# Performance work log

Hardware: AMD Instinct MI355X
Metric: run time of the kernel (lower is better)

## Reference

```python
import jax, jax.numpy as jnp
import numpy as np

B, NF, T, N = 64, 64, 8192, 1024  # batch, n_formants, frames, tokens


def setup_inputs() -> dict:
    key = jax.random.key(0)
    kx, kd = jax.random.split(key)
    x = jax.random.normal(kx, (B, NF, T), dtype=jnp.float32)
    # durations: nonneg ints whose cumsum stays within [0, T]
    ends = jnp.sort(jax.random.randint(kd, (B, N), 0, T + 1), axis=1)
    durations = jnp.diff(ends, axis=1, prepend=jnp.zeros((B, 1), dtype=ends.dtype)).astype(jnp.int64)
    return {"x": x, "durations": durations}


def reference(x, durations):
    # x: [B, NF, T], durations: [B, N]
    dce = jnp.cumsum(durations, axis=1).astype(jnp.int32)          # [B, N] segment ends
    dcs = jnp.pad(dce[:, :-1], ((0, 0), (1, 0)))                   # [B, N] segment starts
    # padded inclusive cumsums along time -> exclusive prefix sums of length T+1
    x_cums = jnp.pad(jnp.cumsum(x, axis=2), ((0, 0), (0, 0), (1, 0)))                    # [B, NF, T+1]
    x_nz_cums = jnp.pad(jnp.cumsum((x != 0.0).astype(x.dtype), axis=2), ((0, 0), (0, 0), (1, 0)))
    b, nf, n = x.shape[0], x.shape[1], durations.shape[1]
    dce_b = jnp.broadcast_to(dce[:, None, :], (b, nf, n))
    dcs_b = jnp.broadcast_to(dcs[:, None, :], (b, nf, n))
    x_sums = jnp.take_along_axis(x_cums, dce_b, axis=2) - jnp.take_along_axis(x_cums, dcs_b, axis=2)
    x_nelems = jnp.take_along_axis(x_nz_cums, dce_b, axis=2) - jnp.take_along_axis(x_nz_cums, dcs_b, axis=2)
    return jnp.where(x_nelems == 0.0, x_nelems, x_sums / x_nelems)  # [B, NF, N]
```

## Files before the change

### kernel.cpp

```cpp
#include <hip/hip_runtime.h>

#define BB 64
#define NF 64
#define TT 8192
#define NN 1024

__global__ __launch_bounds__(NN) void scan_kernel(const int* __restrict__ dur,
                                                  int* __restrict__ bnd) {
    const int b = blockIdx.x;
    const int t = threadIdx.x;
    __shared__ int s[NN];
    s[t] = dur[b * NN + t];
    __syncthreads();
    for (int off = 1; off < NN; off <<= 1) {
        int v = (t >= off) ? s[t - off] : 0;
        __syncthreads();
        s[t] += v;
        __syncthreads();
    }
    bnd[b * (NN + 1) + t + 1] = s[t];
    if (t == 0) bnd[b * (NN + 1)] = 0;
}

__global__ __launch_bounds__(256) void avg_kernel(const float* __restrict__ x,
                                                  const int* __restrict__ bnd,
                                                  float* __restrict__ out) {
    const int row = blockIdx.x;
    const int b   = row / NF;
    const int t   = threadIdx.x;

    __shared__ float xs[TT];
    __shared__ int   bs[NN + 1];

    for (int i = t; i < NN + 1; i += 256) bs[i] = bnd[b * (NN + 1) + i];

    const float4* xv  = (const float4*)(x + (size_t)row * TT);
    float4*       xsv = (float4*)xs;
#pragma unroll
    for (int i = 0; i < TT / 4 / 256; ++i) xsv[t + i * 256] = xv[t + i * 256];
    __syncthreads();

    float* orow = out + (size_t)row * NN;
#pragma unroll
    for (int k = 0; k < NN / 256; ++k) {
        const int n  = t + k * 256;
        const int s0 = bs[n];
        const int e0 = bs[n + 1];
        float sum = 0.0f;
        int   cnt = 0;
        for (int i = s0; i < e0; ++i) {
            float v = xs[i];
            sum += v;
            cnt += (v != 0.0f) ? 1 : 0;
        }
        orow[n] = (cnt != 0) ? (sum / (float)cnt) : 0.0f;
    }
}

extern "C" void kernel_launch(void* const* d_in, const int* in_sizes, int n_in,
                              void* d_out, int out_size, void* d_ws, size_t ws_size,
                              hipStream_t stream) {
    const float* x   = (const float*)d_in[0];
    const int*   dur = (const int*)d_in[1];
    float*       out = (float*)d_out;
    int*         bnd = (int*)d_ws;

    scan_kernel<<<BB, NN, 0, stream>>>(dur, bnd);
    avg_kernel<<<BB * NF, 256, 0, stream>>>(x, bnd, out);
}
```

Measured before the change: 210.6 us.

## Replace per-segment serial summation with in-LDS prefix scan and boundary lookups

The averaging kernel used to walk every segment serially, which gave uneven per-thread loop lengths and heavy divergence. It now builds a per-row prefix sum and nonzero count over float4 chunks in shared memory, using padded LDS indexing and wavefront shuffles. Each token boundary is then resolved to a prefix value plus a partial chunk, and every output becomes a difference of two prefixes. This adds synchronisation and a larger LDS footprint, which may lower occupancy. It also changes float summation order, which can cost precision on long prefixes.

```diff
diff --git a/kernel.cpp b/kernel.cpp
--- a/kernel.cpp
+++ b/kernel.cpp
@@ -4,6 +4,9 @@
 #define NF 64
 #define TT 8192
 #define NN 1024
+#define G  (TT / 4)
+#define PAD(c) ((c) + ((c) >> 3))
+#define CSZ (PAD(G) + 1)
 
 __global__ __launch_bounds__(NN) void scan_kernel(const int* __restrict__ dur,
                                                   int* __restrict__ bnd) {
@@ -25,35 +28,84 @@
 __global__ __launch_bounds__(256) void avg_kernel(const float* __restrict__ x,
                                                   const int* __restrict__ bnd,
                                                   float* __restrict__ out) {
-    const int row = blockIdx.x;
-    const int b   = row / NF;
-    const int t   = threadIdx.x;
+    const int row  = blockIdx.x;
+    const int b    = row / NF;
+    const int t    = threadIdx.x;
+    const int lane = t & 63;
+    const int w    = t >> 6;
 
-    __shared__ float xs[TT];
-    __shared__ int   bs[NN + 1];
+    __shared__ float4 xg[G];
+    __shared__ float  csum[CSZ];
+    __shared__ int    ccnt[CSZ];
+    __shared__ float  P[NN + 1];
+    __shared__ float  Kc[NN + 1];
+    __shared__ float  wsumf[4];
+    __shared__ int    wsumi[4];
 
-    for (int i = t; i < NN + 1; i += 256) bs[i] = bnd[b * (NN + 1) + i];
+    const float4* xv = (const float4*)(x + (size_t)row * TT);
+#pragma unroll
+    for (int k = 0; k < G / 256; ++k) {
+        const int c = t + k * 256;
+        float4 v = xv[c];
+        xg[c] = v;
+        csum[PAD(c)] = v.x + v.y + v.z + v.w;
+        ccnt[PAD(c)] = (v.x != 0.f) + (v.y != 0.f) + (v.z != 0.f) + (v.w != 0.f);
+    }
+    __syncthreads();
 
-    const float4* xv  = (const float4*)(x + (size_t)row * TT);
-    float4*       xsv = (float4*)xs;
+    float sv[8]; int cv[8];
+    float fs = 0.f; int cs = 0;
 #pragma unroll
-    for (int i = 0; i < TT / 4 / 256; ++i) xsv[t + i * 256] = xv[t + i * 256];
+    for (int j = 0; j < 8; ++j) {
+        const int c = 8 * t + j;
+        fs += csum[PAD(c)];
+        cs += ccnt[PAD(c)];
+        sv[j] = fs; cv[j] = cs;
+    }
+    float ws = fs; int wc = cs;
+#pragma unroll
+    for (int d = 1; d < 64; d <<= 1) {
+        float uf = __shfl_up(ws, d, 64);
+        int   ui = __shfl_up(wc, d, 64);
+        if (lane >= d) { ws += uf; wc += ui; }
+    }
+    if (lane == 63) { wsumf[w] = ws; wsumi[w] = wc; }
+    __syncthreads();
+    float woff = 0.f; int coff = 0;
+#pragma unroll
+    for (int i = 0; i < 4; ++i) if (i < w) { woff += wsumf[i]; coff += wsumi[i]; }
+    const float base  = woff + (ws - fs);
+    const int   cbase = coff + (wc - cs);
+#pragma unroll
+    for (int j = 0; j < 8; ++j) {
+        const int c = 8 * t + j;
+        csum[PAD(c)] = base  + (j ? sv[j - 1] : 0.f);
+        ccnt[PAD(c)] = cbase + (j ? cv[j - 1] : 0);
+    }
+    if (t == 255) { csum[PAD(G)] = woff + ws; ccnt[PAD(G)] = coff + wc; }
+    __syncthreads();
+
+    const int* brow = bnd + b * (NN + 1);
+    for (int i = t; i <= NN; i += 256) {
+        const int p = brow[i];
+        const int g = p >> 2, r = p & 3;
+        float4 v = xg[g & (G - 1)];
+        float part = 0.f; int pc = 0;
+        if (r > 0) { part += v.x; pc += (v.x != 0.f); }
+        if (r > 1) { part += v.y; pc += (v.y != 0.f); }
+        if (r > 2) { part += v.z; pc += (v.z != 0.f); }
+        P[i]  = csum[PAD(g)] + part;
+        Kc[i] = (float)(ccnt[PAD(g)] + pc);
+    }
     __syncthreads();
 
     float* orow = out + (size_t)row * NN;
 #pragma unroll
     for (int k = 0; k < NN / 256; ++k) {
-        const int n  = t + k * 256;
-        const int s0 = bs[n];
-        const int e0 = bs[n + 1];
-        float sum = 0.0f;
-        int   cnt = 0;
-        for (int i = s0; i < e0; ++i) {
-            float v = xs[i];
-            sum += v;
-            cnt += (v != 0.0f) ? 1 : 0;
-        }
-        orow[n] = (cnt != 0) ? (sum / (float)cnt) : 0.0f;
+        const int n = t + k * 256;
+        const float s = P[n + 1] - P[n];
+        const float c = Kc[n + 1] - Kc[n];
+        orow[n] = (c != 0.f) ? (s / c) : 0.f;
     }
 }
 
```

After: 203.9 us. -3.2%, faster.
